# Kernel optimization log

Measured on AMD Instinct MI355X. Metric: run time of the kernel, lower is better.

The kernel has to match this reference:

```python
import jax, jax.numpy as jnp
import numpy as np

EPS = 1e-5

def _conv(x, w, pad):
    return jax.lax.conv_general_dilated(x, w, (1, 1), pad,
        dimension_numbers=('NCHW', 'OIHW', 'NCHW'))

def _bn_relu(y, g, b):
    # training-mode BatchNorm2d: stats over (N, H, W) per channel
    mean = jnp.mean(y, axis=(0, 2, 3), keepdims=True)
    var = jnp.var(y, axis=(0, 2, 3), keepdims=True)
    yhat = (y - mean) * jax.lax.rsqrt(var + EPS)
    return jax.nn.relu(yhat * g[None, :, None, None] + b[None, :, None, None])


def setup_inputs() -> dict:
    key = jax.random.key(0)
    ks = jax.random.split(key, 12)
    B, Cin, H, W = 4, 256, 64, 64
    Ci = Cin // 4          # inter_channels = 64
    Cq = Ci // 8           # PAM q/k dim = 8
    Cout = 256
    s = 0.05
    return {
        'x':    jax.random.normal(ks[0], (B, Cin, H, W), jnp.float32),
        'w1':   jax.random.normal(ks[1], (Ci, Cin, 3, 3), jnp.float32) * s,
        'bn_g': jnp.ones((Ci,), jnp.float32),
        'bn_b': jnp.zeros((Ci,), jnp.float32),
        'wq':   jax.random.normal(ks[2], (Cq, Ci, 1, 1), jnp.float32) * s,
        'bq':   jax.random.normal(ks[3], (Cq,), jnp.float32) * s,
        'wk':   jax.random.normal(ks[4], (Cq, Ci, 1, 1), jnp.float32) * s,
        'bk':   jax.random.normal(ks[5], (Cq,), jnp.float32) * s,
        'wv':   jax.random.normal(ks[6], (Ci, Ci, 1, 1), jnp.float32) * s,
        'bv':   jax.random.normal(ks[7], (Ci,), jnp.float32) * s,
        'gamma_pam': jnp.float32(0.5) * jnp.ones((1,), jnp.float32),
        'gamma_cam': jnp.float32(0.5) * jnp.ones((1,), jnp.float32),
        'w2':   jax.random.normal(ks[8], (Ci, Ci, 3, 3), jnp.float32) * s,
        'w8':   jax.random.normal(ks[9], (Cout, Ci, 1, 1), jnp.float32) * s,
        'b8':   jax.random.normal(ks[10], (Cout,), jnp.float32) * s,
    }


def reference(x, w1, bn_g, bn_b, wq, bq, wk, bk, wv, bv,
              gamma_pam, gamma_cam, w2, w8, b8):
    B, _, H, W = x.shape
    N = H * W

    # feat1 = relu(bn1(conv1(x))); feat2 is the identical computation -> reuse
    feat1 = _bn_relu(_conv(x, w1, 'SAME'), bn_g, bn_b)   # [B, Ci, H, W]
    Ci = feat1.shape[1]

    # ---- PAM (position attention) ----
    q = _conv(feat1, wq, 'VALID') + bq[None, :, None, None]   # [B, Cq, H, W]
    k = _conv(feat1, wk, 'VALID') + bk[None, :, None, None]
    v = _conv(feat1, wv, 'VALID') + bv[None, :, None, None]   # [B, Ci, H, W]
    qf = q.reshape(B, -1, N)
    kf = k.reshape(B, -1, N)
    vf = v.reshape(B, Ci, N)
    energy = jnp.einsum('bdi,bdj->bij', qf, kf)               # [B, N, N]
    attn = jax.nn.softmax(energy, axis=-1)
    pam = jnp.einsum('bcj,bij->bci', vf, attn).reshape(B, Ci, H, W)
    sa_feat = gamma_pam[0] * pam + feat1

    sa_conv = _bn_relu(_conv(sa_feat, w2, 'SAME'), bn_g, bn_b)

    # ---- CAM (channel attention) ----
    f = feat1.reshape(B, Ci, N)
    ce = jnp.einsum('bcn,bdn->bcd', f, f)                     # [B, Ci, Ci]
    ce_new = jnp.max(ce, axis=-1, keepdims=True) - ce
    cattn = jax.nn.softmax(ce_new, axis=-1)
    cam = jnp.einsum('bcd,bdn->bcn', cattn, f).reshape(B, Ci, H, W)
    sc_feat = gamma_cam[0] * cam + feat1

    sc_conv = _bn_relu(_conv(sc_feat, w2, 'SAME'), bn_g, bn_b)

    feat_sum = sa_conv + sc_conv
    # conv8: Dropout2d (identity at inference) + 1x1 conv
    out = _conv(feat_sum, w8, 'VALID') + b8[None, :, None, None]
    return out
```

## Files before the change

kernel.cpp:

```cpp
#include <hip/hip_runtime.h>
#include <hip/hip_bf16.h>

#define BB   4
#define CIN  256
#define CI   64
#define COUT 256
#define NPIX 4096
#define LOG2E 1.44269504088896340736f

#define B_Y1V    0x0000000u
#define B_FEAT1  0x0400000u
#define B_SA     0x0800000u
#define B_Y2     0x0C00000u
#define B_SACONV 0x1000000u
#define B_Q      0x1400000u
#define B_K      0x1480000u
#define B_ST     0x15A0000u
#define B_CATT   0x15B1000u
#define B_WP1    0x15C1000u
#define B_WP2    0x1610000u
#define B_PL     0x1630000u
#define B_W8P    0x1640000u
#define B_WQKV   0x1648000u
#define B_BALL   0x164B000u

typedef __attribute__((ext_vector_type(8))) short bf16x8;
typedef __attribute__((ext_vector_type(4))) short bf16x4;
typedef __attribute__((ext_vector_type(4))) float f32x4;

__device__ __forceinline__ short f2bs(float f) {
    union { float f; unsigned u; } c; c.f = f;
    unsigned r = c.u + 0x7FFFu + ((c.u >> 16) & 1u);
    return (short)(r >> 16);
}
__device__ __forceinline__ float bs2f(unsigned short s) {
    union { unsigned u; float f; } c; c.u = ((unsigned)s) << 16;
    return c.f;
}
__device__ __forceinline__ int swz(int wp) { return (wp ^ (wp >> 2)) & 3; }

__global__ __launch_bounds__(256) void k_weights(const float* __restrict__ w1,
                                                 const float* __restrict__ w2,
                                                 const float* __restrict__ w8,
                                                 const float* wq, const float* bq,
                                                 const float* wk, const float* bk,
                                                 const float* wv, const float* bv,
                                                 short* wp1, short* wp2, short* w8p,
                                                 short* wall, float* ball,
                                                 float* st, float* pl) {
    int blk = blockIdx.x, t = threadIdx.x;
    if (blk < 576) {
        int idx = blk * 256 + t;
        if (idx < 147456) {
            int cil = idx & 31, co = (idx >> 5) & 63;
            int rest = idx >> 11, tap = rest % 9, ch = rest / 9;
            wp1[idx] = f2bs(w1[co * CIN * 9 + (ch * 32 + cil) * 9 + tap]);
        }
    } else if (blk < 720) {
        int idx = (blk - 576) * 256 + t;
        if (idx < 36864) {
            int cil = idx & 31, co = (idx >> 5) & 63;
            int rest = idx >> 11, tap = rest % 9, ch = rest / 9;
            wp2[idx] = f2bs(w2[co * CI * 9 + (ch * 32 + cil) * 9 + tap]);
        }
    } else if (blk < 784) {
        int idx = (blk - 720) * 256 + t;
        w8p[idx] = f2bs(w8[idx]);
    } else if (blk < 804) {
        int idx = (blk - 784) * 256 + t;
        if (idx < 5120) {
            int co = idx >> 6, ci = idx & 63;
            float v;
            if (co < 8)       v = wq[co * 64 + ci] * LOG2E;
            else if (co < 16) v = wk[(co - 8) * 64 + ci];
            else              v = wv[(co - 16) * 64 + ci];
            wall[idx] = f2bs(v);
        }
        if (idx < 80) {
            float v;
            if (idx < 8)       v = bq[idx] * LOG2E;
            else if (idx < 16) v = bk[idx - 8];
            else               v = bv[idx - 16];
            ball[idx] = v;
        }
    } else if (blk < 806) {
        int idx = (blk - 804) * 256 + t;
        if (idx < 384) st[idx] = 0.f;
    } else {
        int idx = (blk - 806) * 256 + t;
        pl[idx] = 0.f;
    }
}

template<int NCH>
__global__ __launch_bounds__(256) void k_prep(const float* __restrict__ in,
                                              short* __restrict__ out) {
    __shared__ short tl[4][64][34];
    int blk = blockIdx.x;
    int hq = blk & 15;
    int ch = (blk >> 4) % NCH;
    int b  = blk / (16 * NCH);
    int t = threadIdx.x;
    const int CINT = NCH * 32;

    #pragma unroll
    for (int i = 0; i < 32; ++i) {
        int idx = i * 256 + t;
        int w = idx & 63, hh = (idx >> 6) & 3, ci = idx >> 8;
        float v = in[((size_t)(b * CINT + ch * 32 + ci)) * NPIX + (hq * 4 + hh) * 64 + w];
        tl[hh][w][ci] = f2bs(v);
    }
    __syncthreads();
    unsigned* outu = (unsigned*)(out + (((size_t)(b * NCH + ch)) * NPIX + hq * 4 * 64) * 32);
    #pragma unroll
    for (int i = 0; i < 16; ++i) {
        int j = i * 256 + t;
        int cip = j & 15, w = (j >> 4) & 63, hh = j >> 10;
        unsigned v = *(unsigned*)&tl[hh][w][2 * cip];
        outu[(size_t)(hh * 64 + w) * 16 + cip] = v;
    }
}

__global__ __launch_bounds__(256) void k_pamprep(const short* __restrict__ po,
                                                 const float* __restrict__ pl_acc,
                                                 const float* __restrict__ feat1,
                                                 const float* __restrict__ gp,
                                                 short* __restrict__ out) {
    __shared__ short tl[4][64][34];
    int blk = blockIdx.x;
    int hq = blk & 15;
    int ch = (blk >> 4) & 1;
    int b  = blk >> 5;
    int t = threadIdx.x;
    float g = gp[0];

    #pragma unroll
    for (int i = 0; i < 32; ++i) {
        int idx = i * 256 + t;
        int w = idx & 63, hh = (idx >> 6) & 3, ci = idx >> 8;
        int pix = (hq * 4 + hh) * 64 + w;
        size_t o = ((size_t)(b * 64 + ch * 32 + ci)) * NPIX + pix;
        float s = bs2f((unsigned short)po[o])
                + bs2f((unsigned short)po[o + 1048576])
                + bs2f((unsigned short)po[o + 2097152])
                + bs2f((unsigned short)po[o + 3145728]);
        float v = feat1[o] + g * s / pl_acc[b * NPIX + pix];
        tl[hh][w][ci] = f2bs(v);
    }
    __syncthreads();
    unsigned* outu = (unsigned*)(out + (((size_t)(b * 2 + ch)) * NPIX + hq * 4 * 64) * 32);
    #pragma unroll
    for (int i = 0; i < 16; ++i) {
        int j = i * 256 + t;
        int cip = j & 15, w = (j >> 4) & 63, hh = j >> 10;
        unsigned v = *(unsigned*)&tl[hh][w][2 * cip];
        outu[(size_t)(hh * 64 + w) * 16 + cip] = v;
    }
}

template<int NCH>
__device__ __forceinline__ void conv_body(const short* __restrict__ xprep,
                                          const short* __restrict__ wp,
                                          float* __restrict__ y0,
                                          float* __restrict__ y1,
                                          int blk, int t) {
    __shared__ __align__(16) short xl[3][66][32];
    int lane = t & 63, wv = t >> 6;
    int ks = blk >> 8;
    int b = (blk >> 6) & 3, h = blk & 63;
    int g = lane >> 4, n16 = lane & 15;
    constexpr int NH = NCH / 2;
    int c0 = ks * NH;

    if (t < 24) {
        int r = t >> 3, cc = ((t >> 2) & 1) ? 65 : 0, u = t & 3;
        bf16x8 z = {};
        *(bf16x8*)&xl[r][cc][u * 8] = z;
    }

    f32x4 acc[4];
    #pragma unroll
    for (int i = 0; i < 4; ++i) acc[i] = (f32x4){0.f, 0.f, 0.f, 0.f};

    int sw = t >> 2, su = t & 3;
    int spu = su ^ swz(sw + 1);

    for (int ch = c0; ch < c0 + NH; ++ch) {
        __syncthreads();
        #pragma unroll
        for (int r = 0; r < 3; ++r) {
            int hh = h + r - 1;
            bf16x8 v = {};
            if (hh >= 0 && hh < 64)
                v = *(const bf16x8*)(xprep + (((size_t)(b * NCH + ch)) * 64 + hh) * 64 * 32 + sw * 32 + su * 8);
            *(bf16x8*)&xl[r][sw + 1][spu * 8] = v;
        }
        __syncthreads();

        const short* wbase = wp + ((size_t)(ch * 9)) * 64 * 32;
        #pragma unroll
        for (int tap = 0; tap < 9; ++tap) {
            int kr = tap / 3, kc = tap % 3;
            bf16x8 a = *(const bf16x8*)(wbase + ((size_t)(tap * 64 + wv * 16 + n16)) * 32 + g * 8);
            #pragma unroll
            for (int nt = 0; nt < 4; ++nt) {
                int wpix = nt * 16 + n16 + kc;
                int pu = g ^ swz(wpix);
                bf16x8 bx = *(const bf16x8*)&xl[kr][wpix][pu * 8];
                acc[nt] = __builtin_amdgcn_mfma_f32_16x16x32_bf16(a, bx, acc[nt], 0, 0, 0);
            }
        }
    }

    float* y = ks ? y1 : y0;
    #pragma unroll
    for (int nt = 0; nt < 4; ++nt) {
        #pragma unroll
        for (int r = 0; r < 4; ++r) {
            int co = wv * 16 + g * 4 + r;
            y[((size_t)(b * CI + co)) * NPIX + h * 64 + nt * 16 + n16] = acc[nt][r];
        }
    }
}

template<int NCH>
__global__ __launch_bounds__(256) void k_convmfma(const short* __restrict__ xprep,
                                                  const short* __restrict__ wp,
                                                  float* __restrict__ y0,
                                                  float* __restrict__ y1) {
    conv_body<NCH>(xprep, wp, y0, y1, blockIdx.x, threadIdx.x);
}

__global__ __launch_bounds__(256) void k_conv2x(const short* __restrict__ inA,
                                                const short* __restrict__ inB,
                                                const short* __restrict__ wp,
                                                float* a0, float* a1,
                                                float* b0, float* b1) {
    int blk = blockIdx.x;
    int w = blk >> 9;
    conv_body<2>(w ? inB : inA, wp, w ? b0 : a0, w ? b1 : a1, blk & 511, threadIdx.x);
}

__device__ __forceinline__ void bnstats_body(const float* __restrict__ y0,
                                             const float* __restrict__ y1,
                                             float* stats, int blk, int t) {
    int c = blk >> 2, b = blk & 3;
    size_t base = ((size_t)(b * 64 + c)) * NPIX;
    float s = 0.f, sq = 0.f;
    for (int i = t; i < NPIX; i += 256) {
        float v = y0[base + i] + y1[base + i];
        s += v; sq += v * v;
    }
    __shared__ float rs[8];
    for (int o = 32; o; o >>= 1) { s += __shfl_down(s, o); sq += __shfl_down(sq, o); }
    if ((t & 63) == 0) { rs[t >> 6] = s; rs[4 + (t >> 6)] = sq; }
    __syncthreads();
    if (t == 0) {
        atomicAdd(&stats[c], rs[0] + rs[1] + rs[2] + rs[3]);
        atomicAdd(&stats[64 + c], rs[4] + rs[5] + rs[6] + rs[7]);
    }
}

__global__ __launch_bounds__(256) void k_bnstats(const float* y0, const float* y1, float* stats) {
    bnstats_body(y0, y1, stats, blockIdx.x, threadIdx.x);
}
__global__ __launch_bounds__(256) void k_bnstats2x(const float* a0, const float* a1,
                                                   const float* b0, const float* b1,
                                                   float* sta, float* stb) {
    int blk = blockIdx.x;
    int w = blk >> 8;
    bnstats_body(w ? b0 : a0, w ? b1 : a1, w ? stb : sta, blk & 255, threadIdx.x);
}

__device__ __forceinline__ void bnapply_body(const float* y0, const float* y1,
                                             const float* stats, const float* g,
                                             const float* bta, float* out, int i) {
    int c = (i >> 12) & 63;
    float mean = stats[c] * (1.f / 16384.f);
    float var = stats[64 + c] * (1.f / 16384.f) - mean * mean;
    float rs = rsqrtf(var + 1e-5f);
    float v = (y0[i] + y1[i] - mean) * rs * g[c] + bta[c];
    out[i] = v > 0.f ? v : 0.f;
}

__global__ __launch_bounds__(256) void k_bnapply2(const float* y0, const float* y1,
                                                  const float* stats, const float* g,
                                                  const float* bta, float* out) {
    bnapply_body(y0, y1, stats, g, bta, out, blockIdx.x * 256 + threadIdx.x);
}
__global__ __launch_bounds__(256) void k_bnapply2x(const float* a0, const float* a1,
                                                   const float* b0, const float* b1,
                                                   const float* sta, const float* stb,
                                                   const float* g, const float* bta,
                                                   float* oa, float* ob) {
    int blk = blockIdx.x;
    int w = blk >> 12;
    int i = (blk & 4095) * 256 + threadIdx.x;
    bnapply_body(w ? b0 : a0, w ? b1 : a1, w ? stb : sta, g, bta, w ? ob : oa, i);
}

__global__ __launch_bounds__(256) void k_qkvmfma(const float* __restrict__ feat1,
                                                 const short* __restrict__ wall,
                                                 const float* __restrict__ ball,
                                                 short* __restrict__ q,
                                                 short* __restrict__ k,
                                                 short* __restrict__ v) {
    __shared__ __align__(16) short fl[64][64];
    int t = threadIdx.x;
    int lane = t & 63, wv = t >> 6;
    int blk = blockIdx.x;
    int h = blk & 63, b = blk >> 6;
    int n16 = lane & 15, g = lane >> 4;

    {
        int n = t & 63, ug2 = t >> 6;
        const float* fp = feat1 + ((size_t)b * CI) * NPIX + h * 64 + n;
        #pragma unroll
        for (int uu = 0; uu < 2; ++uu) {
            int u = ug2 + uu * 4;
            int ci0 = u * 8;
            short tmp[8];
            #pragma unroll
            for (int j = 0; j < 8; ++j) tmp[j] = f2bs(fp[(size_t)(ci0 + j) * NPIX]);
            int phys = u ^ (n & 7);
            *(bf16x8*)&fl[n][phys * 8] = *(bf16x8*)tmp;
        }
    }
    __syncthreads();

    f32x4 acc[4];
    #pragma unroll
    for (int i = 0; i < 4; ++i) acc[i] = (f32x4){0.f, 0.f, 0.f, 0.f};
    f32x4 acc4 = (f32x4){0.f, 0.f, 0.f, 0.f};

    #pragma unroll
    for (int kc = 0; kc < 2; ++kc) {
        bf16x8 a = *(const bf16x8*)&wall[(size_t)(wv * 16 + n16) * 64 + kc * 32 + g * 8];
        bf16x8 a4 = *(const bf16x8*)&wall[(size_t)(64 + n16) * 64 + kc * 32 + g * 8];
        #pragma unroll
        for (int nt = 0; nt < 4; ++nt) {
            int n = nt * 16 + n16;
            int phys = (kc * 4 + g) ^ (n & 7);
            bf16x8 bx = *(const bf16x8*)&fl[n][phys * 8];
            acc[nt] = __builtin_amdgcn_mfma_f32_16x16x32_bf16(a, bx, acc[nt], 0, 0, 0);
            if (nt == wv) acc4 = __builtin_amdgcn_mfma_f32_16x16x32_bf16(a4, bx, acc4, 0, 0, 0);
        }
    }

    #pragma unroll
    for (int nt = 0; nt < 4; ++nt) {
        int pix = h * 64 + nt * 16 + n16;
        #pragma unroll
        for (int r = 0; r < 4; ++r) {
            int co = wv * 16 + g * 4 + r;
            short val = f2bs(acc[nt][r] + ball[co]);
            if (co < 8)       q[((size_t)(b * 8 + co)) * NPIX + pix] = val;
            else if (co < 16) k[((size_t)(b * 8 + co - 8)) * NPIX + pix] = val;
            else              v[((size_t)(b * 64 + co - 16)) * NPIX + pix] = val;
        }
    }
    {
        int pix = h * 64 + wv * 16 + n16;
        #pragma unroll
        for (int r = 0; r < 4; ++r) {
            int co = 64 + g * 4 + r;
            v[((size_t)(b * 64 + co - 16)) * NPIX + pix] = f2bs(acc4[r] + ball[co]);
        }
    }
}

__global__ __launch_bounds__(256) void k_pampart(const short* __restrict__ q,
                                                 const short* __restrict__ k,
                                                 const short* __restrict__ v,
                                                 short* __restrict__ po,
                                                 float* __restrict__ pl_acc) {
    __shared__ __align__(16) short kl[128][16];
    __shared__ __align__(16) short pl[64][136];

    int t = threadIdx.x;
    int lane = t & 63, w = t >> 6;
    int blk = blockIdx.x;
    int jc = blk >> 8, b = (blk >> 6) & 3, ic = blk & 63;
    int i0 = ic * 64;
    int n16 = lane & 15, g = lane >> 4;

    const short* qb = q + (size_t)b * 8 * NPIX;
    const short* kb = k + (size_t)b * 8 * NPIX;
    const short* vb = v + (size_t)b * 64 * NPIX;

    #pragma unroll
    for (int i = 0; i < 2; ++i) {
        int idx = i * 256 + t;
        int jj = idx & 127, dz = 8 + ((idx >> 7) << 1);
        *(unsigned*)&kl[jj][dz] = 0u;
    }

    bf16x8 aq = {};
    if (lane < 16) {
        int irow = i0 + w * 16 + lane;
        #pragma unroll
        for (int e = 0; e < 8; ++e) aq[e] = qb[(size_t)e * NPIX + irow];
    }

    f32x4 acc[4];
    #pragma unroll
    for (int i = 0; i < 4; ++i) acc[i] = (f32x4){0.f, 0.f, 0.f, 0.f};
    float lacc = 0.f;
    const f32x4 zz = {0.f, 0.f, 0.f, 0.f};

    for (int ro = 0; ro < 8; ++ro) {
        int j0 = jc * 1024 + ro * 128;
        #pragma unroll
        for (int i = 0; i < 2; ++i) {
            int idx = i * 256 + t;
            int jj = idx & 127, dp2 = idx >> 7;
            unsigned lo = (unsigned short)kb[(size_t)(dp2 * 2) * NPIX + j0 + jj];
            unsigned hi = (unsigned short)kb[(size_t)(dp2 * 2 + 1) * NPIX + j0 + jj];
            *(unsigned*)&kl[jj][dp2 * 2] = lo | (hi << 16);
        }
        bf16x8 av[4];
        #pragma unroll
        for (int ks = 0; ks < 4; ++ks)
            av[ks] = *(const bf16x8*)&vb[(size_t)(w * 16 + n16) * NPIX + j0 + ks * 32 + g * 8];
        __syncthreads();

        #pragma unroll
        for (int jsub = 0; jsub < 8; ++jsub) {
            bf16x8 bk = {};
            if (lane < 32)
                bk = *(const bf16x8*)&kl[jsub * 16 + n16][g * 8];
            f32x4 s = __builtin_amdgcn_mfma_f32_16x16x32_bf16(bk, aq, zz, 0, 0, 0);
            float e0 = exp2f(s[0]), e1 = exp2f(s[1]), e2 = exp2f(s[2]), e3 = exp2f(s[3]);
            lacc += (e0 + e1) + (e2 + e3);
            bf16x4 pk = { f2bs(e0), f2bs(e1), f2bs(e2), f2bs(e3) };
            *(bf16x4*)&pl[w * 16 + n16][jsub * 16 + g * 4] = pk;
        }
        __syncthreads();

        #pragma unroll
        for (int isub = 0; isub < 4; ++isub) {
            #pragma unroll
            for (int ks = 0; ks < 4; ++ks) {
                bf16x8 bp = *(const bf16x8*)&pl[isub * 16 + n16][ks * 32 + g * 8];
                acc[isub] = __builtin_amdgcn_mfma_f32_16x16x32_bf16(av[ks], bp, acc[isub], 0, 0, 0);
            }
        }
        __syncthreads();
    }

    {
        float lv = lacc;
        lv += __shfl_xor(lv, 16);
        lv += __shfl_xor(lv, 32);
        if (lane < 16)
            atomicAdd(&pl_acc[b * NPIX + i0 + w * 16 + lane], lv);
    }

    #pragma unroll
    for (int isub = 0; isub < 4; ++isub) {
        #pragma unroll
        for (int r = 0; r < 4; ++r) {
            int c = w * 16 + g * 4 + r;
            size_t o = ((size_t)((jc * BB + b) * 64 + c)) * NPIX + i0 + isub * 16 + n16;
            po[o] = f2bs(acc[isub][r]);
        }
    }
}

__global__ __launch_bounds__(256) void k_grampart(const float* __restrict__ f,
                                                  float* __restrict__ gp) {
    __shared__ __align__(16) float fl[64 * 68];
    int blk = blockIdx.x;
    int b = blk >> 6, nc = blk & 63;
    int n0 = nc * 64;
    int t = threadIdx.x;
    int c = t & 63, dg = t >> 6;
    float acc[16];
    #pragma unroll
    for (int i = 0; i < 16; ++i) acc[i] = 0.f;
    for (int idx = t; idx < 4096; idx += 256) {
        int cc = idx >> 6, nn = idx & 63;
        fl[nn * 68 + cc] = f[((size_t)b * 64 + cc) * NPIX + n0 + nn];
    }
    __syncthreads();
    for (int nn = 0; nn < 64; ++nn) {
        float fc = fl[nn * 68 + c];
        const float4* fd = (const float4*)(fl + nn * 68 + dg * 16);
        #pragma unroll
        for (int k4 = 0; k4 < 4; ++k4) {
            float4 vv = fd[k4];
            acc[k4 * 4 + 0] += fc * vv.x;
            acc[k4 * 4 + 1] += fc * vv.y;
            acc[k4 * 4 + 2] += fc * vv.z;
            acc[k4 * 4 + 3] += fc * vv.w;
        }
    }
    float* dst = gp + (size_t)nc * 16384 + ((size_t)b * 64 + c) * 64 + dg * 16;
    #pragma unroll
    for (int kk = 0; kk < 16; ++kk) dst[kk] = acc[kk];
}

__global__ void k_camsm2(const float* __restrict__ gp, float* __restrict__ cattn) {
    int row = blockIdx.x;
    int d = threadIdx.x;
    float v = 0.f;
    #pragma unroll 8
    for (int p = 0; p < 64; ++p) v += gp[(size_t)p * 16384 + row * 64 + d];
    float mn = v;
    for (int s = 32; s; s >>= 1) mn = fminf(mn, __shfl_xor(mn, s));
    float e = exp2f((mn - v) * LOG2E);
    float sum = e;
    for (int s = 32; s; s >>= 1) sum += __shfl_xor(sum, s);
    cattn[(size_t)row * 64 + d] = e / sum;
}

__global__ __launch_bounds__(256) void k_cam(const float* __restrict__ cattn,
                                             const float* __restrict__ f,
                                             const float* __restrict__ gcp,
                                             float* __restrict__ sc) {
    __shared__ __align__(16) float Al[64 * 68];
    __shared__ float fl[64 * 64];
    int blk = blockIdx.x;
    int b = blk >> 6, nc = blk & 63;
    int n0 = nc * 64;
    int t = threadIdx.x;
    int nl = t & 63, cg = t >> 6;
    for (int idx = t; idx < 4096; idx += 256) {
        int cc = idx >> 6, dd = idx & 63;
        Al[dd * 68 + cc] = cattn[((size_t)b * 64 + cc) * 64 + dd];
    }
    for (int idx = t; idx < 4096; idx += 256) {
        int dd = idx >> 6, nn = idx & 63;
        fl[dd * 64 + nn] = f[((size_t)b * 64 + dd) * NPIX + n0 + nn];
    }
    __syncthreads();
    float acc[16];
    #pragma unroll
    for (int i = 0; i < 16; ++i) acc[i] = 0.f;
    for (int d = 0; d < 64; ++d) {
        float fv = fl[d * 64 + nl];
        const float4* A4 = (const float4*)(Al + d * 68 + cg * 16);
        #pragma unroll
        for (int k4 = 0; k4 < 4; ++k4) {
            float4 a = A4[k4];
            acc[k4 * 4 + 0] += a.x * fv;
            acc[k4 * 4 + 1] += a.y * fv;
            acc[k4 * 4 + 2] += a.z * fv;
            acc[k4 * 4 + 3] += a.w * fv;
        }
    }
    float g = gcp[0];
    #pragma unroll
    for (int kk = 0; kk < 16; ++kk) {
        int c = cg * 16 + kk;
        size_t o = ((size_t)b * 64 + c) * NPIX + n0 + nl;
        sc[o] = g * acc[kk] + f[o];
    }
}

__global__ __launch_bounds__(256) void k_finalmfma(const float* __restrict__ sa,
                                                   const float* __restrict__ sc,
                                                   const short* __restrict__ w8p,
                                                   const float* __restrict__ b8,
                                                   float* __restrict__ out) {
    __shared__ __align__(16) short fl[64][64];
    int t = threadIdx.x;
    int lane = t & 63, wv = t >> 6;
    int blk = blockIdx.x;
    int h = blk & 63, b = (blk >> 6) & 3, cq = blk >> 8;
    int n16 = lane & 15, g = lane >> 4;

    {
        int n = t & 63, ug2 = t >> 6;
        const float* sap = sa + ((size_t)b * CI) * NPIX + h * 64 + n;
        const float* scp = sc + ((size_t)b * CI) * NPIX + h * 64 + n;
        #pragma unroll
        for (int uu = 0; uu < 2; ++uu) {
            int u = ug2 + uu * 4;
            int ci0 = u * 8;
            short tmp[8];
            #pragma unroll
            for (int j = 0; j < 8; ++j) {
                size_t o = (size_t)(ci0 + j) * NPIX;
                tmp[j] = f2bs(sap[o] + scp[o]);
            }
            int phys = u ^ (n & 7);
            *(bf16x8*)&fl[n][phys * 8] = *(bf16x8*)tmp;
        }
    }
    __syncthreads();

    f32x4 acc[4];
    #pragma unroll
    for (int i = 0; i < 4; ++i) acc[i] = (f32x4){0.f, 0.f, 0.f, 0.f};
    int cobase = cq * 64 + wv * 16;

    #pragma unroll
    for (int kc = 0; kc < 2; ++kc) {
        bf16x8 a = *(const bf16x8*)&w8p[(size_t)(cobase + n16) * 64 + kc * 32 + g * 8];
        #pragma unroll
        for (int nt = 0; nt < 4; ++nt) {
            int n = nt * 16 + n16;
            int phys = (kc * 4 + g) ^ (n & 7);
            bf16x8 bx = *(const bf16x8*)&fl[n][phys * 8];
            acc[nt] = __builtin_amdgcn_mfma_f32_16x16x32_bf16(a, bx, acc[nt], 0, 0, 0);
        }
    }

    #pragma unroll
    for (int nt = 0; nt < 4; ++nt) {
        #pragma unroll
        for (int r = 0; r < 4; ++r) {
            int co = cobase + g * 4 + r;
            out[((size_t)(b * COUT + co)) * NPIX + h * 64 + nt * 16 + n16] = acc[nt][r] + b8[co];
        }
    }
}

extern "C" void kernel_launch(void* const* d_in, const int* in_sizes, int n_in,
                              void* d_out, int out_size, void* d_ws, size_t ws_size,
                              hipStream_t stream) {
    (void)in_sizes; (void)n_in; (void)out_size; (void)ws_size;
    const float* x    = (const float*)d_in[0];
    const float* w1   = (const float*)d_in[1];
    const float* bng  = (const float*)d_in[2];
    const float* bnb  = (const float*)d_in[3];
    const float* wq   = (const float*)d_in[4];
    const float* bq   = (const float*)d_in[5];
    const float* wk   = (const float*)d_in[6];
    const float* bk   = (const float*)d_in[7];
    const float* wv   = (const float*)d_in[8];
    const float* bv   = (const float*)d_in[9];
    const float* gpam = (const float*)d_in[10];
    const float* gcam = (const float*)d_in[11];
    const float* w2   = (const float*)d_in[12];
    const float* w8   = (const float*)d_in[13];
    const float* b8   = (const float*)d_in[14];
    float* out = (float*)d_out;

    char* WB = (char*)d_ws;
    float* fC1P0   = (float*)(WB + B_Y1V);
    float* fC1P1   = (float*)(WB + B_SACONV);
    float* fGP     = (float*)(WB + B_Y1V);
    short* fV      = (short*)(WB + B_Y1V);
    short* fSPREPSC= (short*)(WB + B_Y1V + 0x200000);
    short* fSAPREP = (short*)(WB + B_Y1V);
    float* fFEAT1  = (float*)(WB + B_FEAT1);
    short* fXPREP  = (short*)(WB + B_SA);
    float* fSCFEAT = (float*)(WB + B_SA);
    float* fC2B1   = (float*)(WB + B_SA);
    short* fPO     = (short*)(WB + B_Y2);
    float* fC2A0   = (float*)(WB + B_Y2);
    float* fC2B0   = (float*)(WB + B_FEAT1);
    float* fC2A1   = (float*)(WB + B_SACONV);
    short* fQ      = (short*)(WB + B_Q);
    short* fK      = (short*)(WB + B_K);
    float* fST     = (float*)(WB + B_ST);
    float* fST2a   = fST + 128;
    float* fST2b   = fST + 256;
    float* fCATT   = (float*)(WB + B_CATT);
    short* fWP1    = (short*)(WB + B_WP1);
    short* fWP2    = (short*)(WB + B_WP2);
    float* fPL     = (float*)(WB + B_PL);
    short* fW8P    = (short*)(WB + B_W8P);
    short* fWQKV   = (short*)(WB + B_WQKV);
    float* fBALL   = (float*)(WB + B_BALL);

    k_weights<<<870, 256, 0, stream>>>(w1, w2, w8, wq, bq, wk, bk, wv, bv,
                                       fWP1, fWP2, fW8P, fWQKV, fBALL, fST, fPL);

    k_prep<8><<<512, 256, 0, stream>>>(x, fXPREP);
    k_convmfma<8><<<512, 256, 0, stream>>>(fXPREP, fWP1, fC1P0, fC1P1);
    k_bnstats<<<256, 256, 0, stream>>>(fC1P0, fC1P1, fST);
    k_bnapply2<<<4096, 256, 0, stream>>>(fC1P0, fC1P1, fST, bng, bnb, fFEAT1);

    k_grampart<<<256, 256, 0, stream>>>(fFEAT1, fGP);
    k_camsm2<<<256, 64, 0, stream>>>(fGP, fCATT);
    k_cam<<<256, 256, 0, stream>>>(fCATT, fFEAT1, gcam, fSCFEAT);
    k_prep<2><<<128, 256, 0, stream>>>(fSCFEAT, fSPREPSC);

    k_qkvmfma<<<256, 256, 0, stream>>>(fFEAT1, fWQKV, fBALL, fQ, fK, fV);
    k_pampart<<<1024, 256, 0, stream>>>(fQ, fK, fV, fPO, fPL);
    k_pamprep<<<128, 256, 0, stream>>>(fPO, fPL, fFEAT1, gpam, fSAPREP);

    k_conv2x<<<1024, 256, 0, stream>>>(fSAPREP, fSPREPSC, fWP2, fC2A0, fC2A1, fC2B0, fC2B1);
    k_bnstats2x<<<512, 256, 0, stream>>>(fC2A0, fC2A1, fC2B0, fC2B1, fST2a, fST2b);
    k_bnapply2x<<<8192, 256, 0, stream>>>(fC2A0, fC2A1, fC2B0, fC2B1, fST2a, fST2b,
                                          bng, bnb, fC2A1, fC2B1);

    k_finalmfma<<<1024, 256, 0, stream>>>(fC2A1, fC2B1, fW8P, b8, out);
}
```

Before: 146.4 us.

## Merge independent launches and widen PAM key tiles with swizzled LDS

Independent kernels are merged into single launches via blockIdx dispatch: weight packing with input prep, QKV projection with the Gram partials, and the CAM prep with the PAM prep. This cuts launch count and lets small grids share the GPU. The PAM partial kernel now handles 256 keys per outer step instead of 128 and drops the zero-padded K layout, so the QK MFMA reads only 8 real dims. P writes and reads now go through an XOR-swizzled LDS layout to avoid bank conflicts. The Gram partial buffer moves to a different workspace region so it no longer aliases V, and LDS use and register pressure per block grow.

```diff
diff --git a/kernel.cpp b/kernel.cpp
--- a/kernel.cpp
+++ b/kernel.cpp
@@ -39,16 +39,16 @@
 }
 __device__ __forceinline__ int swz(int wp) { return (wp ^ (wp >> 2)) & 3; }
 
-__global__ __launch_bounds__(256) void k_weights(const float* __restrict__ w1,
-                                                 const float* __restrict__ w2,
-                                                 const float* __restrict__ w8,
-                                                 const float* wq, const float* bq,
-                                                 const float* wk, const float* bk,
-                                                 const float* wv, const float* bv,
-                                                 short* wp1, short* wp2, short* w8p,
-                                                 short* wall, float* ball,
-                                                 float* st, float* pl) {
-    int blk = blockIdx.x, t = threadIdx.x;
+
+__device__ __forceinline__ void weights_body(const float* __restrict__ w1,
+                                             const float* __restrict__ w2,
+                                             const float* __restrict__ w8,
+                                             const float* wq, const float* bq,
+                                             const float* wk, const float* bk,
+                                             const float* wv, const float* bv,
+                                             short* wp1, short* wp2, short* w8p,
+                                             short* wall, float* ball,
+                                             float* st, float* pl, int blk, int t) {
     if (blk < 576) {
         int idx = blk * 256 + t;
         if (idx < 147456) {
@@ -93,14 +93,12 @@
 }
 
 template<int NCH>
-__global__ __launch_bounds__(256) void k_prep(const float* __restrict__ in,
-                                              short* __restrict__ out) {
+__device__ __forceinline__ void prep_body(const float* __restrict__ in,
+                                          short* __restrict__ out, int blk, int t) {
     __shared__ short tl[4][64][34];
-    int blk = blockIdx.x;
     int hq = blk & 15;
     int ch = (blk >> 4) % NCH;
     int b  = blk / (16 * NCH);
-    int t = threadIdx.x;
     const int CINT = NCH * 32;
 
     #pragma unroll
@@ -121,17 +119,30 @@
     }
 }
 
-__global__ __launch_bounds__(256) void k_pamprep(const short* __restrict__ po,
-                                                 const float* __restrict__ pl_acc,
-                                                 const float* __restrict__ feat1,
-                                                 const float* __restrict__ gp,
-                                                 short* __restrict__ out) {
+__global__ __launch_bounds__(256) void k_prepw(const float* __restrict__ x,
+                                               const float* w1, const float* w2, const float* w8,
+                                               const float* wq, const float* bq,
+                                               const float* wk, const float* bk,
+                                               const float* wv, const float* bv,
+                                               short* xprep,
+                                               short* wp1, short* wp2, short* w8p,
+                                               short* wall, float* ball,
+                                               float* st, float* pl) {
+    int blk = blockIdx.x, t = threadIdx.x;
+    if (blk < 512) prep_body<8>(x, xprep, blk, t);
+    else weights_body(w1, w2, w8, wq, bq, wk, bk, wv, bv,
+                      wp1, wp2, w8p, wall, ball, st, pl, blk - 512, t);
+}
+
+__device__ __forceinline__ void pamprep_body(const short* __restrict__ po,
+                                             const float* __restrict__ pl_acc,
+                                             const float* __restrict__ feat1,
+                                             const float* __restrict__ gp,
+                                             short* __restrict__ out, int blk, int t) {
     __shared__ short tl[4][64][34];
-    int blk = blockIdx.x;
     int hq = blk & 15;
     int ch = (blk >> 4) & 1;
     int b  = blk >> 5;
-    int t = threadIdx.x;
     float g = gp[0];
 
     #pragma unroll
@@ -156,6 +167,18 @@
         unsigned v = *(unsigned*)&tl[hh][w][2 * cip];
         outu[(size_t)(hh * 64 + w) * 16 + cip] = v;
     }
+}
+
+__global__ __launch_bounds__(256) void k_preppam(const float* __restrict__ scfeat,
+                                                 short* __restrict__ sprep_sc,
+                                                 const short* __restrict__ po,
+                                                 const float* __restrict__ pl_acc,
+                                                 const float* __restrict__ feat1,
+                                                 const float* __restrict__ gp,
+                                                 short* __restrict__ saprep) {
+    int blk = blockIdx.x, t = threadIdx.x;
+    if (blk < 128) prep_body<2>(scfeat, sprep_sc, blk, t);
+    else pamprep_body(po, pl_acc, feat1, gp, saprep, blk - 128, t);
 }
 
 template<int NCH>
@@ -299,16 +322,14 @@
     bnapply_body(w ? b0 : a0, w ? b1 : a1, w ? stb : sta, g, bta, w ? ob : oa, i);
 }
 
-__global__ __launch_bounds__(256) void k_qkvmfma(const float* __restrict__ feat1,
-                                                 const short* __restrict__ wall,
-                                                 const float* __restrict__ ball,
-                                                 short* __restrict__ q,
-                                                 short* __restrict__ k,
-                                                 short* __restrict__ v) {
+__device__ __forceinline__ void qkv_body(const float* __restrict__ feat1,
+                                         const short* __restrict__ wall,
+                                         const float* __restrict__ ball,
+                                         short* __restrict__ q,
+                                         short* __restrict__ k,
+                                         short* __restrict__ v, int blk, int t) {
     __shared__ __align__(16) short fl[64][64];
-    int t = threadIdx.x;
     int lane = t & 63, wv = t >> 6;
-    int blk = blockIdx.x;
     int h = blk & 63, b = blk >> 6;
     int n16 = lane & 15, g = lane >> 4;
 
@@ -369,13 +390,54 @@
     }
 }
 
+__device__ __forceinline__ void gram_body(const float* __restrict__ f,
+                                          float* __restrict__ gp, int blk, int t) {
+    __shared__ __align__(16) float fl[64 * 68];
+    int b = blk >> 6, nc = blk & 63;
+    int n0 = nc * 64;
+    int c = t & 63, dg = t >> 6;
+    float acc[16];
+    #pragma unroll
+    for (int i = 0; i < 16; ++i) acc[i] = 0.f;
+    for (int idx = t; idx < 4096; idx += 256) {
+        int cc = idx >> 6, nn = idx & 63;
+        fl[nn * 68 + cc] = f[((size_t)b * 64 + cc) * NPIX + n0 + nn];
+    }
+    __syncthreads();
+    for (int nn = 0; nn < 64; ++nn) {
+        float fc = fl[nn * 68 + c];
+        const float4* fd = (const float4*)(fl + nn * 68 + dg * 16);
+        #pragma unroll
+        for (int k4 = 0; k4 < 4; ++k4) {
+            float4 vv = fd[k4];
+            acc[k4 * 4 + 0] += fc * vv.x;
+            acc[k4 * 4 + 1] += fc * vv.y;
+            acc[k4 * 4 + 2] += fc * vv.z;
+            acc[k4 * 4 + 3] += fc * vv.w;
+        }
+    }
+    float* dst = gp + (size_t)nc * 16384 + ((size_t)b * 64 + c) * 64 + dg * 16;
+    #pragma unroll
+    for (int kk = 0; kk < 16; ++kk) dst[kk] = acc[kk];
+}
+
+__global__ __launch_bounds__(256) void k_qkvgram(const float* __restrict__ feat1,
+                                                 const short* __restrict__ wall,
+                                                 const float* __restrict__ ball,
+                                                 short* q, short* k, short* v,
+                                                 float* gp) {
+    int blk = blockIdx.x, t = threadIdx.x;
+    if (blk < 256) qkv_body(feat1, wall, ball, q, k, v, blk, t);
+    else gram_body(feat1, gp, blk - 256, t);
+}
+
 __global__ __launch_bounds__(256) void k_pampart(const short* __restrict__ q,
                                                  const short* __restrict__ k,
                                                  const short* __restrict__ v,
                                                  short* __restrict__ po,
                                                  float* __restrict__ pl_acc) {
-    __shared__ __align__(16) short kl[128][16];
-    __shared__ __align__(16) short pl[64][136];
+    __shared__ __align__(16) short kl[256][8];
+    __shared__ __align__(16) short pl[64][272];
 
     int t = threadIdx.x;
     int lane = t & 63, w = t >> 6;
@@ -383,18 +445,12 @@
     int jc = blk >> 8, b = (blk >> 6) & 3, ic = blk & 63;
     int i0 = ic * 64;
     int n16 = lane & 15, g = lane >> 4;
+    int key = n16 & 7;
 
     const short* qb = q + (size_t)b * 8 * NPIX;
     const short* kb = k + (size_t)b * 8 * NPIX;
     const short* vb = v + (size_t)b * 64 * NPIX;
 
-    #pragma unroll
-    for (int i = 0; i < 2; ++i) {
-        int idx = i * 256 + t;
-        int jj = idx & 127, dz = 8 + ((idx >> 7) << 1);
-        *(unsigned*)&kl[jj][dz] = 0u;
-    }
-
     bf16x8 aq = {};
     if (lane < 16) {
         int irow = i0 + w * 16 + lane;
@@ -408,40 +464,41 @@
     float lacc = 0.f;
     const f32x4 zz = {0.f, 0.f, 0.f, 0.f};
 
-    for (int ro = 0; ro < 8; ++ro) {
-        int j0 = jc * 1024 + ro * 128;
-        #pragma unroll
-        for (int i = 0; i < 2; ++i) {
-            int idx = i * 256 + t;
-            int jj = idx & 127, dp2 = idx >> 7;
-            unsigned lo = (unsigned short)kb[(size_t)(dp2 * 2) * NPIX + j0 + jj];
-            unsigned hi = (unsigned short)kb[(size_t)(dp2 * 2 + 1) * NPIX + j0 + jj];
-            *(unsigned*)&kl[jj][dp2 * 2] = lo | (hi << 16);
-        }
-        bf16x8 av[4];
-        #pragma unroll
-        for (int ks = 0; ks < 4; ++ks)
+    for (int ro = 0; ro < 4; ++ro) {
+        int j0 = jc * 1024 + ro * 256;
+        #pragma unroll
+        for (int it = 0; it < 4; ++it) {
+            int idx = it * 256 + t;
+            int row = idx >> 2, col = idx & 3;
+            unsigned lo = (unsigned short)kb[(size_t)(2 * col) * NPIX + j0 + row];
+            unsigned hi = (unsigned short)kb[(size_t)(2 * col + 1) * NPIX + j0 + row];
+            *(unsigned*)&kl[row][col * 2] = lo | (hi << 16);
+        }
+        bf16x8 av[8];
+        #pragma unroll
+        for (int ks = 0; ks < 8; ++ks)
             av[ks] = *(const bf16x8*)&vb[(size_t)(w * 16 + n16) * NPIX + j0 + ks * 32 + g * 8];
         __syncthreads();
 
         #pragma unroll
-        for (int jsub = 0; jsub < 8; ++jsub) {
+        for (int jsub = 0; jsub < 16; ++jsub) {
             bf16x8 bk = {};
-            if (lane < 32)
-                bk = *(const bf16x8*)&kl[jsub * 16 + n16][g * 8];
+            if (lane < 16) bk = *(const bf16x8*)&kl[jsub * 16 + n16][0];
             f32x4 s = __builtin_amdgcn_mfma_f32_16x16x32_bf16(bk, aq, zz, 0, 0, 0);
             float e0 = exp2f(s[0]), e1 = exp2f(s[1]), e2 = exp2f(s[2]), e3 = exp2f(s[3]);
             lacc += (e0 + e1) + (e2 + e3);
             bf16x4 pk = { f2bs(e0), f2bs(e1), f2bs(e2), f2bs(e3) };
-            *(bf16x4*)&pl[w * 16 + n16][jsub * 16 + g * 4] = pk;
+            int uw = (jsub * 2 + (g >> 1)) ^ key;
+            *(bf16x4*)&pl[w * 16 + n16][uw * 8 + (g & 1) * 4] = pk;
         }
         __syncthreads();
 
         #pragma unroll
         for (int isub = 0; isub < 4; ++isub) {
             #pragma unroll
-            for (int ks = 0; ks < 4; ++ks) {
-                bf16x8 bp = *(const bf16x8*)&pl[isub * 16 + n16][ks * 32 + g * 8];
+            for (int ks = 0; ks < 8; ++ks) {
+                int ur = (ks * 4 + g) ^ key;
+                bf16x8 bp = *(const bf16x8*)&pl[isub * 16 + n16][ur * 8];
                 acc[isub] = __builtin_amdgcn_mfma_f32_16x16x32_bf16(av[ks], bp, acc[isub], 0, 0, 0);
             }
         }
@@ -465,39 +522,6 @@
             po[o] = f2bs(acc[isub][r]);
         }
     }
-}
-
-__global__ __launch_bounds__(256) void k_grampart(const float* __restrict__ f,
-                                                  float* __restrict__ gp) {
-    __shared__ __align__(16) float fl[64 * 68];
-    int blk = blockIdx.x;
-    int b = blk >> 6, nc = blk & 63;
-    int n0 = nc * 64;
-    int t = threadIdx.x;
-    int c = t & 63, dg = t >> 6;
-    float acc[16];
-    #pragma unroll
-    for (int i = 0; i < 16; ++i) acc[i] = 0.f;
-    for (int idx = t; idx < 4096; idx += 256) {
-        int cc = idx >> 6, nn = idx & 63;
-        fl[nn * 68 + cc] = f[((size_t)b * 64 + cc) * NPIX + n0 + nn];
-    }
-    __syncthreads();
-    for (int nn = 0; nn < 64; ++nn) {
-        float fc = fl[nn * 68 + c];
-        const float4* fd = (const float4*)(fl + nn * 68 + dg * 16);
-        #pragma unroll
-        for (int k4 = 0; k4 < 4; ++k4) {
-            float4 vv = fd[k4];
-            acc[k4 * 4 + 0] += fc * vv.x;
-            acc[k4 * 4 + 1] += fc * vv.y;
-            acc[k4 * 4 + 2] += fc * vv.z;
-            acc[k4 * 4 + 3] += fc * vv.w;
-        }
-    }
-    float* dst = gp + (size_t)nc * 16384 + ((size_t)b * 64 + c) * 64 + dg * 16;
-    #pragma unroll
-    for (int kk = 0; kk < 16; ++kk) dst[kk] = acc[kk];
 }
 
 __global__ void k_camsm2(const float* __restrict__ gp, float* __restrict__ cattn) {
@@ -641,7 +665,7 @@
     char* WB = (char*)d_ws;
     float* fC1P0   = (float*)(WB + B_Y1V);
     float* fC1P1   = (float*)(WB + B_SACONV);
-    float* fGP     = (float*)(WB + B_Y1V);
+    float* fGP     = (float*)(WB + B_SACONV);
     short* fV      = (short*)(WB + B_Y1V);
     short* fSPREPSC= (short*)(WB + B_Y1V + 0x200000);
     short* fSAPREP = (short*)(WB + B_Y1V);
@@ -666,22 +690,19 @@
     short* fWQKV   = (short*)(WB + B_WQKV);
     float* fBALL   = (float*)(WB + B_BALL);
 
-    k_weights<<<870, 256, 0, stream>>>(w1, w2, w8, wq, bq, wk, bk, wv, bv,
-                                       fWP1, fWP2, fW8P, fWQKV, fBALL, fST, fPL);
-
-    k_prep<8><<<512, 256, 0, stream>>>(x, fXPREP);
+    k_prepw<<<1382, 256, 0, stream>>>(x, w1, w2, w8, wq, bq, wk, bk, wv, bv,
+                                      fXPREP, fWP1, fWP2, fW8P, fWQKV, fBALL, fST, fPL);
+
     k_convmfma<8><<<512, 256, 0, stream>>>(fXPREP, fWP1, fC1P0, fC1P1);
     k_bnstats<<<256, 256, 0, stream>>>(fC1P0, fC1P1, fST);
     k_bnapply2<<<4096, 256, 0, stream>>>(fC1P0, fC1P1, fST, bng, bnb, fFEAT1);
 
-    k_grampart<<<256, 256, 0, stream>>>(fFEAT1, fGP);
+    k_qkvgram<<<512, 256, 0, stream>>>(fFEAT1, fWQKV, fBALL, fQ, fK, fV, fGP);
     k_camsm2<<<256, 64, 0, stream>>>(fGP, fCATT);
+
+    k_pampart<<<1024, 256, 0, stream>>>(fQ, fK, fV, fPO, fPL);
     k_cam<<<256, 256, 0, stream>>>(fCATT, fFEAT1, gcam, fSCFEAT);
-    k_prep<2><<<128, 256, 0, stream>>>(fSCFEAT, fSPREPSC);
-
-    k_qkvmfma<<<256, 256, 0, stream>>>(fFEAT1, fWQKV, fBALL, fQ, fK, fV);
-    k_pampart<<<1024, 256, 0, stream>>>(fQ, fK, fV, fPO, fPL);
-    k_pamprep<<<128, 256, 0, stream>>>(fPO, fPL, fFEAT1, gpam, fSAPREP);
+    k_preppam<<<256, 256, 0, stream>>>(fSCFEAT, fSPREPSC, fPO, fPL, fFEAT1, gpam, fSAPREP);
 
     k_conv2x<<<1024, 256, 0, stream>>>(fSAPREP, fSPREPSC, fWP2, fC2A0, fC2A1, fC2B0, fC2B1);
     k_bnstats2x<<<512, 256, 0, stream>>>(fC2A0, fC2A1, fC2B0, fC2B1, fST2a, fST2b);
```

Result: slower. 149.5 us (+2.1%).
